# Performance work log

Hardware: AMD Instinct MI355X
Metric: run time of the kernel (lower is better)

## Reference

```python
import jax, jax.numpy as jnp
import numpy as np

BSZ, SEQ, DIM, NH = 2, 2048, 2048, 16
HD = DIM // NH  # 128


def setup_inputs() -> dict:
    key = jax.random.key(0)
    ks = jax.random.split(key, 6)
    x = jax.random.normal(ks[0], (BSZ, SEQ, DIM), dtype=jnp.float32)
    # torch Linear weights: [out_features, in_features]
    scale = 1.0 / np.sqrt(DIM)
    wq = jax.random.normal(ks[1], (DIM, DIM), dtype=jnp.float32) * scale
    wk = jax.random.normal(ks[2], (DIM, DIM), dtype=jnp.float32) * scale
    wv = jax.random.normal(ks[3], (DIM, DIM), dtype=jnp.float32) * scale
    wo = jax.random.normal(ks[4], (DIM, DIM), dtype=jnp.float32) * scale
    # RoPE freqs (llama style): theta=10000
    inv_freq = 1.0 / (10000.0 ** (jnp.arange(0, HD, 2, dtype=jnp.float32) / HD))  # [HD//2]
    t = jnp.arange(SEQ, dtype=jnp.float32)
    angles = jnp.outer(t, inv_freq)  # [SEQ, HD//2]
    freqs_cos = jnp.cos(angles)
    freqs_sin = jnp.sin(angles)
    # causal additive mask [SEQ, SEQ]
    mask = jnp.where(jnp.tril(jnp.ones((SEQ, SEQ), dtype=bool)), 0.0, -jnp.inf).astype(jnp.float32)
    return {"x": x, "wq": wq, "wk": wk, "wv": wv, "wo": wo,
            "freqs_cos": freqs_cos, "freqs_sin": freqs_sin, "mask": mask}


def _apply_rope(v, cos, sin):
    # v: [b, s, h, hd]; complex pairs are interleaved (even=real, odd=imag)
    b, s, h, hd = v.shape
    vr = v.reshape(b, s, h, hd // 2, 2)
    v0, v1 = vr[..., 0], vr[..., 1]
    c = cos[None, :, None, :]  # [1, s, 1, hd//2]
    sn = sin[None, :, None, :]
    out = jnp.stack([v0 * c - v1 * sn, v0 * sn + v1 * c], axis=-1)
    return out.reshape(b, s, h, hd)


def reference(x, wq, wk, wv, wo, freqs_cos, freqs_sin, mask):
    b, s, _ = x.shape
    xq = (x @ wq.T).reshape(b, s, NH, HD)
    xk = (x @ wk.T).reshape(b, s, NH, HD)
    xv = (x @ wv.T).reshape(b, s, NH, HD)
    xq = _apply_rope(xq, freqs_cos, freqs_sin)
    xk = _apply_rope(xk, freqs_cos, freqs_sin)
    # [b, h, s, s]
    scores = jnp.einsum('bqhd,bkhd->bhqk', xq, xk) / jnp.sqrt(jnp.float32(HD))
    scores = scores + mask[None, None, :, :]
    probs = jax.nn.softmax(scores.astype(jnp.float32), axis=-1).astype(scores.dtype)
    out = jnp.einsum('bhqk,bkhd->bqhd', probs, xv).reshape(b, s, NH * HD)
    return out @ wo.T
```

## Files before the change

### kernel.cpp

```cpp
#include <hip/hip_runtime.h>
#include <hip/hip_bf16.h>
#include <stdint.h>

typedef __bf16 bf16x8 __attribute__((ext_vector_type(8)));
typedef float f32x4 __attribute__((ext_vector_type(4)));
typedef unsigned short u16;
typedef unsigned int u32;

#define DEVI __device__ __forceinline__

DEVI u16 f2b(float f){ __bf16 h = (__bf16)f; return __builtin_bit_cast(u16, h); }
DEVI float b2f(u16 u){ return (float)__builtin_bit_cast(__bf16, u); }

constexpr int BSZ = 2, SEQ = 2048, DIM = 2048, NH = 16, HD = 128;

#if defined(__has_builtin)
#if __has_builtin(__builtin_amdgcn_global_load_lds)
#define HAVE_ASYNC_LDS 1
#endif
#endif

DEVI void cp16(void* lds, const void* g){
#ifdef HAVE_ASYNC_LDS
  auto gp = (const __attribute__((address_space(1))) u32*)(uintptr_t)g;
  auto lp = (__attribute__((address_space(3))) u32*)(uintptr_t)lds;
  __builtin_amdgcn_global_load_lds(gp, lp, 16, 0, 0);
#else
  *(uint4*)lds = *(const uint4*)g;
#endif
}

__global__ __launch_bounds__(256) void k_convert(
    const float* __restrict__ x, const float* __restrict__ wq,
    const float* __restrict__ wk, const float* __restrict__ wv,
    const float* __restrict__ wo,
    u16* __restrict__ xb, u16* __restrict__ wqkv, u16* __restrict__ wob)
{
  int e = (blockIdx.x * 256 + threadIdx.x) * 4;
  float4 v; u16* dp;
  if (e < 8388608){
    v = *(const float4*)&x[e]; dp = &xb[e];
  } else if (e < 20971520){
    int o = e - 8388608; int sec = o >> 22; int oo = o & 4194303;
    const float* w = (sec == 0) ? wq : ((sec == 1) ? wk : wv);
    v = *(const float4*)&w[oo]; dp = &wqkv[o];
  } else {
    int o = e - 20971520;
    v = *(const float4*)&wo[o]; dp = &wob[o];
  }
  ushort4 r; r.x = f2b(v.x); r.y = f2b(v.y); r.z = f2b(v.z); r.w = f2b(v.w);
  *(ushort4*)dp = r;
}

__global__ __launch_bounds__(256) void k_gemm_qkv(
    const u16* __restrict__ A, const u16* __restrict__ W,
    const float* __restrict__ fc, const float* __restrict__ fs,
    u16* __restrict__ Qd, u16* __restrict__ Kd, u16* __restrict__ Vd)
{
  __shared__ u16 As[128*32];
  __shared__ u16 Bs[128*32];
  __shared__ u16 Cs[128*136];
  const int t = threadIdx.x;
  const int lane = t & 63;
  const int l15 = lane & 15, quad = lane >> 4;
  const int wave = t >> 6;
  const int wr = (wave >> 1) * 64, wc = (wave & 1) * 64;
  const int tm = blockIdx.y * 128, tn = blockIdx.x * 128;
  const int arow = t >> 2, acol = (t & 3) * 8;

  f32x4 acc[4][4] = {};
  for (int k0 = 0; k0 < DIM; k0 += 32){
    __syncthreads();
    #pragma unroll
    for (int is = 0; is < 2; ++is){
      int row = is*64 + arow;
      cp16(&As[is*2048 + t*8], &A[(size_t)(tm + row)*DIM + k0 + acol]);
      cp16(&Bs[is*2048 + t*8], &W[(size_t)(tn + row)*DIM + k0 + acol]);
    }
    __syncthreads();
    bf16x8 af[4], bfr[4];
    #pragma unroll
    for (int i = 0; i < 4; ++i){
      af[i]  = *(const bf16x8*)&As[(wr + i*16 + l15)*32 + quad*8];
      bfr[i] = *(const bf16x8*)&Bs[(wc + i*16 + l15)*32 + quad*8];
    }
    #pragma unroll
    for (int mt = 0; mt < 4; ++mt)
      #pragma unroll
      for (int nt = 0; nt < 4; ++nt)
        acc[mt][nt] = __builtin_amdgcn_mfma_f32_16x16x32_bf16(af[mt], bfr[nt], acc[mt][nt], 0, 0, 0);
  }
  #pragma unroll
  for (int mt = 0; mt < 4; ++mt)
    #pragma unroll
    for (int nt = 0; nt < 4; ++nt)
      #pragma unroll
      for (int r = 0; r < 4; ++r)
        Cs[(wr + mt*16 + quad*4 + r)*136 + wc + nt*16 + l15] = f2b(acc[mt][nt][r]);
  __syncthreads();

  const int sec = tn >> 11;
  const int hh = (tn & 2047) >> 7;
  u16* dst = (sec == 0) ? Qd : ((sec == 1) ? Kd : Vd);
  const float qs = (sec == 0) ? (0.08838834764831845f * 1.4426950408889634f) : 1.0f;
  const int col0 = (t & 15) * 8;
  #pragma unroll
  for (int jj = 0; jj < 8; ++jj){
    int row = (t >> 4) + jj*16;
    int m = tm + row;
    int b = m >> 11, s = m & 2047;
    uint4 cv = *(const uint4*)&Cs[row*136 + col0];
    const u16* cp = (const u16*)&cv;
    u16 op[8];
    if (sec < 2){
      float4 c4 = *(const float4*)&fc[(size_t)s*64 + (col0 >> 1)];
      float4 s4 = *(const float4*)&fs[(size_t)s*64 + (col0 >> 1)];
      float cc[4] = {c4.x*qs, c4.y*qs, c4.z*qs, c4.w*qs};
      float ss[4] = {s4.x*qs, s4.y*qs, s4.z*qs, s4.w*qs};
      #pragma unroll
      for (int p = 0; p < 4; ++p){
        float a = b2f(cp[2*p]), bb = b2f(cp[2*p+1]);
        op[2*p]   = f2b(a*cc[p] - bb*ss[p]);
        op[2*p+1] = f2b(a*ss[p] + bb*cc[p]);
      }
    } else {
      #pragma unroll
      for (int p = 0; p < 8; ++p) op[p] = cp[p];
    }
    *(uint4*)&dst[((size_t)(b*NH + hh)*SEQ + s)*HD + col0] = *(const uint4*)op;
  }
}

__global__ __launch_bounds__(256) void k_vtrans(
    const u16* __restrict__ V, u16* __restrict__ Vt)
{
  __shared__ u16 ts[64*72];
  const int t = threadIdx.x;
  const int st = blockIdx.x, dt = blockIdx.y, bh = blockIdx.z;
  const size_t base  = (size_t)bh * SEQ * HD;
  const size_t baseT = (size_t)bh * HD * SEQ;
  #pragma unroll
  for (int i = 0; i < 2; ++i){
    int s = i*32 + (t>>3), c = t&7;
    *(uint4*)&ts[s*72 + c*8] = *(const uint4*)&V[base + (size_t)(st*64 + s)*HD + dt*64 + c*8];
  }
  __syncthreads();
  #pragma unroll
  for (int i = 0; i < 2; ++i){
    int d = i*32 + (t>>3), sc = t&7;
    u16 tmp[8];
    #pragma unroll
    for (int j = 0; j < 8; ++j) tmp[j] = ts[(sc*8 + j)*72 + d];
    *(uint4*)&Vt[baseT + (size_t)(dt*64 + d)*SEQ + st*64 + sc*8] = *(const uint4*)tmp;
  }
}

__global__ __launch_bounds__(512) void k_flash(
    const u16* __restrict__ Qd, const u16* __restrict__ Kd,
    const u16* __restrict__ Vt, u16* __restrict__ OP0, u16* __restrict__ OP1,
    float* __restrict__ Mp, float* __restrict__ Lp)
{
  __shared__ u16 Ks[64*136];
  __shared__ u16 Vs[128*72];
  __shared__ u16 Ps[8*16*72];

  const int t = threadIdx.x, lane = t & 63, wave = t >> 6;
  const int l15 = lane & 15, quad = lane >> 4;
  const int j = blockIdx.x >> 1, split = blockIdx.x & 1;
  const int h = blockIdx.y, b = blockIdx.z, bh = b*NH + h;
  const size_t base  = (size_t)bh * SEQ * HD;
  const size_t baseT = (size_t)bh * HD * SEQ;
  u16* Psw = &Ps[wave*16*72];
  u16* OPs = split ? OP1 : OP0;
  const int lo = 17*split, hi = lo + 17;
  const int qt0 = j, qt1 = 15 - j;
  const int len0 = 2*qt0 + 2;

  const int krow = t >> 4, kcol = (t & 15) * 8;
  const int vrow = t >> 3, vcol = (t & 7) * 8;

  for (int pass = 0; pass < 2; ++pass){
    const int qt = pass ? qt1 : qt0;
    const int len = 2*qt + 2;
    int kt0 = pass ? (lo - len0) : lo; if (kt0 < 0) kt0 = 0;
    int kt1 = pass ? (hi - len0) : hi; if (kt1 > len) kt1 = len;
    const int qb = qt*128 + wave*16;

    bf16x8 qf[4];
    #pragma unroll
    for (int ks = 0; ks < 4; ++ks)
      qf[ks] = *(const bf16x8*)&Qd[base + (size_t)(qb + l15)*HD + ks*32 + quad*8];

    f32x4 oacc[8] = {};
    float m_s = -1e30f, l_s = 0.f;

    if (kt0 < kt1){
      uint4 kreg[2], vreg[2];
      #pragma unroll
      for (int i = 0; i < 2; ++i){
        kreg[i] = *(const uint4*)&Kd[base + (size_t)(kt0*64 + i*32 + krow)*HD + kcol];
        vreg[i] = *(const uint4*)&Vt[baseT + (size_t)(i*64 + vrow)*SEQ + kt0*64 + vcol];
      }
      for (int kt = kt0; kt < kt1; ++kt){
        __syncthreads();
        #pragma unroll
        for (int i = 0; i < 2; ++i){
          *(uint4*)&Ks[(i*32 + krow)*136 + kcol] = kreg[i];
          *(uint4*)&Vs[(i*64 + vrow)*72 + vcol] = vreg[i];
        }
        __syncthreads();
        if (kt + 1 < kt1){
          #pragma unroll
          for (int i = 0; i < 2; ++i){
            kreg[i] = *(const uint4*)&Kd[base + (size_t)((kt+1)*64 + i*32 + krow)*HD + kcol];
            vreg[i] = *(const uint4*)&Vt[baseT + (size_t)(i*64 + vrow)*SEQ + (kt+1)*64 + vcol];
          }
        }
        if (kt*64 <= qb + 15){
          f32x4 sacc[4] = {};
          #pragma unroll
          for (int ks = 0; ks < 4; ++ks){
            bf16x8 kf[4];
            #pragma unroll
            for (int nk = 0; nk < 4; ++nk)
              kf[nk] = *(const bf16x8*)&Ks[(nk*16 + l15)*136 + ks*32 + quad*8];
            #pragma unroll
            for (int nk = 0; nk < 4; ++nk)
              sacc[nk] = __builtin_amdgcn_mfma_f32_16x16x32_bf16(kf[nk], qf[ks], sacc[nk], 0, 0, 0);
          }
          if (kt*64 + 63 > qb){
            int q = qb + l15;
            #pragma unroll
            for (int nk = 0; nk < 4; ++nk)
              #pragma unroll
              for (int r = 0; r < 4; ++r){
                int key = kt*64 + nk*16 + quad*4 + r;
                if (key > q) sacc[nk][r] = -1e30f;
              }
          }
          float m4[4];
          #pragma unroll
          for (int nk = 0; nk < 4; ++nk)
            m4[nk] = fmaxf(fmaxf(sacc[nk][0], sacc[nk][1]), fmaxf(sacc[nk][2], sacc[nk][3]));
          float rm = fmaxf(fmaxf(m4[0], m4[1]), fmaxf(m4[2], m4[3]));
          rm = fmaxf(rm, __shfl_xor(rm, 16));
          rm = fmaxf(rm, __shfl_xor(rm, 32));
          float mnew = fmaxf(m_s, rm);
          float alpha = exp2f(m_s - mnew);
          m_s = mnew;
          float s4[4];
          #pragma unroll
          for (int nk = 0; nk < 4; ++nk){
            u16 pk[4];
            float p0 = exp2f(sacc[nk][0] - mnew);
            float p1 = exp2f(sacc[nk][1] - mnew);
            float p2 = exp2f(sacc[nk][2] - mnew);
            float p3 = exp2f(sacc[nk][3] - mnew);
            pk[0] = f2b(p0); pk[1] = f2b(p1); pk[2] = f2b(p2); pk[3] = f2b(p3);
            s4[nk] = (p0 + p1) + (p2 + p3);
            *(uint2*)&Psw[l15*72 + nk*16 + quad*4] = *(const uint2*)pk;
          }
          float rs = (s4[0] + s4[1]) + (s4[2] + s4[3]);
          rs += __shfl_xor(rs, 16);
          rs += __shfl_xor(rs, 32);
          l_s = l_s*alpha + rs;
          #pragma unroll
          for (int db = 0; db < 8; ++db)
            #pragma unroll
            for (int r = 0; r < 4; ++r) oacc[db][r] *= alpha;
          #pragma unroll
          for (int k2 = 0; k2 < 2; ++k2){
            bf16x8 pf = *(const bf16x8*)&Psw[l15*72 + k2*32 + quad*8];
            #pragma unroll
            for (int db = 0; db < 8; ++db){
              bf16x8 vf = *(const bf16x8*)&Vs[(db*16 + l15)*72 + k2*32 + quad*8];
              oacc[db] = __builtin_amdgcn_mfma_f32_16x16x32_bf16(vf, pf, oacc[db], 0, 0, 0);
            }
          }
        }
      }
    }
    {
      int s = qb + l15;
      #pragma unroll
      for (int db = 0; db < 8; ++db){
        u16 ok[4];
        #pragma unroll
        for (int r = 0; r < 4; ++r) ok[r] = f2b(oacc[db][r]);
        *(uint2*)&OPs[(((size_t)(b*SEQ + s))*NH + h)*HD + db*16 + quad*4] = *(const uint2*)ok;
      }
      if (quad == 0){
        size_t mi = ((size_t)split*BSZ*NH + bh)*SEQ + s;
        Mp[mi] = m_s;
        Lp[mi] = l_s;
      }
    }
  }
}

__global__ __launch_bounds__(256) void k_combine(
    u16* __restrict__ OP0, const u16* __restrict__ OP1,
    const float* __restrict__ Mp, const float* __restrict__ Lp)
{
  size_t flat = ((size_t)blockIdx.x*256 + threadIdx.x)*8;
  int h = (int)((flat >> 7) & 15);
  int s = (int)((flat >> 11) & 2047);
  int b = (int)(flat >> 22);
  size_t row = ((size_t)(b*NH + h))*SEQ + s;
  const size_t off1 = (size_t)BSZ*NH*SEQ;
  float m0 = Mp[row], l0 = Lp[row];
  float m1 = Mp[row + off1], l1 = Lp[row + off1];
  float m = fmaxf(m0, m1);
  float w0 = exp2f(m0 - m), w1 = exp2f(m1 - m);
  float inv = 1.0f / (w0*l0 + w1*l1);
  uint4 a = *(const uint4*)&OP0[flat];
  uint4 c = *(const uint4*)&OP1[flat];
  const u16* pa = (const u16*)&a;
  const u16* pc = (const u16*)&c;
  u16 o[8];
  #pragma unroll
  for (int i = 0; i < 8; ++i)
    o[i] = f2b((b2f(pa[i])*w0 + b2f(pc[i])*w1) * inv);
  *(uint4*)&OP0[flat] = *(const uint4*)o;
}

__global__ __launch_bounds__(256) void k_gemm_out(
    const u16* __restrict__ A, const u16* __restrict__ W, float* __restrict__ out)
{
  __shared__ u16 As[128*32];
  __shared__ u16 Bs[128*32];
  const int t = threadIdx.x;
  const int lane = t & 63;
  const int l15 = lane & 15, quad = lane >> 4;
  const int wave = t >> 6;
  const int wr = (wave >> 1) * 64, wc = (wave & 1) * 64;
  const int tm = blockIdx.y * 128, tn = blockIdx.x * 128;
  const int arow = t >> 2, acol = (t & 3) * 8;

  f32x4 acc[4][4] = {};
  for (int k0 = 0; k0 < DIM; k0 += 32){
    __syncthreads();
    #pragma unroll
    for (int is = 0; is < 2; ++is){
      int row = is*64 + arow;
      cp16(&As[is*2048 + t*8], &A[(size_t)(tm + row)*DIM + k0 + acol]);
      cp16(&Bs[is*2048 + t*8], &W[(size_t)(tn + row)*DIM + k0 + acol]);
    }
    __syncthreads();
    bf16x8 af[4], bfr[4];
    #pragma unroll
    for (int i = 0; i < 4; ++i){
      af[i]  = *(const bf16x8*)&As[(wr + i*16 + l15)*32 + quad*8];
      bfr[i] = *(const bf16x8*)&Bs[(wc + i*16 + l15)*32 + quad*8];
    }
    #pragma unroll
    for (int mt = 0; mt < 4; ++mt)
      #pragma unroll
      for (int nt = 0; nt < 4; ++nt)
        acc[mt][nt] = __builtin_amdgcn_mfma_f32_16x16x32_bf16(af[mt], bfr[nt], acc[mt][nt], 0, 0, 0);
  }
  #pragma unroll
  for (int mt = 0; mt < 4; ++mt)
    #pragma unroll
    for (int nt = 0; nt < 4; ++nt)
      #pragma unroll
      for (int r = 0; r < 4; ++r){
        int row = tm + wr + mt*16 + quad*4 + r;
        int col = tn + wc + nt*16 + l15;
        out[(size_t)row*DIM + col] = acc[mt][nt][r];
      }
}

extern "C" void kernel_launch(void* const* d_in, const int* in_sizes, int n_in,
                              void* d_out, int out_size, void* d_ws, size_t ws_size,
                              hipStream_t stream)
{
  const float* x  = (const float*)d_in[0];
  const float* wq = (const float*)d_in[1];
  const float* wk = (const float*)d_in[2];
  const float* wv = (const float*)d_in[3];
  const float* wo = (const float*)d_in[4];
  const float* fc = (const float*)d_in[5];
  const float* fs = (const float*)d_in[6];
  float* out = (float*)d_out;

  char* ws = (char*)d_ws;
  u16* xb   = (u16*)(ws);
  u16* wqkv = (u16*)(ws + 16777216);
  u16* wob  = (u16*)(ws + 41943040);
  u16* Qr   = (u16*)(ws + 50331648);
  u16* Kr   = (u16*)(ws + 67108864);
  u16* Vr   = (u16*)(ws + 83886080);
  u16* Ob   = (u16*)(ws + 100663296);
  u16* VtT  = xb;
  u16* OP1  = wqkv;
  float* Mp = (float*)(ws + 33554432);
  float* Lp = (float*)(ws + 34078720);

  k_convert <<<24576, 256, 0, stream>>>(x, wq, wk, wv, wo, xb, wqkv, wob);
  k_gemm_qkv<<<dim3(48, 32), 256, 0, stream>>>(xb, wqkv, fc, fs, Qr, Kr, Vr);
  k_vtrans  <<<dim3(32, 2, 32), 256, 0, stream>>>(Vr, VtT);
  k_flash   <<<dim3(16, NH, BSZ), 512, 0, stream>>>(Qr, Kr, VtT, Ob, OP1, Mp, Lp);
  k_combine <<<4096, 256, 0, stream>>>(Ob, OP1, Mp, Lp);
  k_gemm_out<<<dim3(16, 32), 256, 0, stream>>>(Ob, wob, out);
}
```

Baseline: 467.2 us.

## Rewrite projection GEMMs with 256x128 tiles, double-buffered K=64 staging and swizzled LDS

Both projection GEMMs now share one core with 256x128 tiles on 512 threads. Global-to-LDS copies are double-buffered over K steps of 64, which removes one barrier per iteration and overlaps loads with MFMA work. LDS is XOR-swizzled to avoid bank conflicts, MFMA bursts are raised in priority, and block ids are remapped so neighbouring workgroups share input tiles in cache. The output GEMM launches only 256 blocks, which may underfill the GPU and hurt occupancy.

New measurement: 434.5 us. 7.0% less time.

```diff
diff --git a/kernel.cpp b/kernel.cpp
--- a/kernel.cpp
+++ b/kernel.cpp
@@ -52,51 +52,92 @@
   *(ushort4*)dp = r;
 }
 
-__global__ __launch_bounds__(256) void k_gemm_qkv(
+DEVI void gemm_core_256x128(u16* smem, const u16* __restrict__ A, const u16* __restrict__ B,
+                            int tm, int tn, int t, f32x4 (&acc)[4][4])
+{
+  const int lane = t & 63, l15 = lane & 15, quad = lane >> 4;
+  const int wave = t >> 6, wm = wave >> 1, wn = wave & 1;
+  const int swr = (l15 & 7) << 3;
+  const int rb = t >> 3;
+  const int csw = ((t & 7) ^ (rb & 7)) << 3;
+  const u16* As0 = A + (size_t)(tm + rb) * DIM + csw;
+  const u16* Bs0 = B + (size_t)(tn + rb) * DIM + csw;
+
+  auto STAGE = [&](int kt){
+    const int buf = kt & 1;
+    const int kb = kt * 64;
+    u16* d = &smem[buf * 24576 + t * 8];
+    #pragma unroll
+    for (int p = 0; p < 4; ++p)
+      cp16(d + p * 4096, As0 + (size_t)p * (64 * DIM) + kb);
+    #pragma unroll
+    for (int p = 0; p < 2; ++p)
+      cp16(d + 16384 + p * 4096, Bs0 + (size_t)p * (64 * DIM) + kb);
+  };
+
+  STAGE(0);
+  #pragma unroll 2
+  for (int kt = 0; kt < DIM / 64; ++kt){
+    __syncthreads();
+    if (kt < DIM / 64 - 1) STAGE(kt + 1);
+    const u16* Ab = &smem[(kt & 1) * 24576];
+    const u16* Bb = Ab + 16384;
+    bf16x8 Af[4][2], Bf[4][2];
+    #pragma unroll
+    for (int mt = 0; mt < 4; ++mt)
+      #pragma unroll
+      for (int ks = 0; ks < 2; ++ks)
+        Af[mt][ks] = *(const bf16x8*)&Ab[(wm * 64 + mt * 16 + l15) * 64 + ((ks * 32 + quad * 8) ^ swr)];
+    #pragma unroll
+    for (int nt = 0; nt < 4; ++nt)
+      #pragma unroll
+      for (int ks = 0; ks < 2; ++ks)
+        Bf[nt][ks] = *(const bf16x8*)&Bb[(wn * 64 + nt * 16 + l15) * 64 + ((ks * 32 + quad * 8) ^ swr)];
+    #pragma unroll
+    for (int c = 0; c < 4; ++c){
+      const int mb = (c >> 1) * 2, nb = (c & 1) * 2;
+      __builtin_amdgcn_s_setprio(1);
+      #pragma unroll
+      for (int mi = 0; mi < 2; ++mi)
+        #pragma unroll
+        for (int ni = 0; ni < 2; ++ni)
+          #pragma unroll
+          for (int ks = 0; ks < 2; ++ks)
+            acc[mb + mi][nb + ni] = __builtin_amdgcn_mfma_f32_16x16x32_bf16(
+                Af[mb + mi][ks], Bf[nb + ni][ks], acc[mb + mi][nb + ni], 0, 0, 0);
+      __builtin_amdgcn_s_setprio(0);
+    }
+  }
+  __syncthreads();
+}
+
+__global__ __launch_bounds__(512, 2) void k_gemm_qkv(
     const u16* __restrict__ A, const u16* __restrict__ W,
     const float* __restrict__ fc, const float* __restrict__ fs,
     u16* __restrict__ Qd, u16* __restrict__ Kd, u16* __restrict__ Vd)
 {
-  __shared__ u16 As[128*32];
-  __shared__ u16 Bs[128*32];
-  __shared__ u16 Cs[128*136];
+  __shared__ __align__(16) u16 smem[49152];
   const int t = threadIdx.x;
-  const int lane = t & 63;
-  const int l15 = lane & 15, quad = lane >> 4;
-  const int wave = t >> 6;
-  const int wr = (wave >> 1) * 64, wc = (wave & 1) * 64;
-  const int tm = blockIdx.y * 128, tn = blockIdx.x * 128;
-  const int arow = t >> 2, acol = (t & 3) * 8;
-
+  const int wg = blockIdx.x;
+  const int id = (wg & 7) * 96 + (wg >> 3);
+  const int tm = (id & 15) << 8;
+  const int tn = (id >> 4) << 7;
   f32x4 acc[4][4] = {};
-  for (int k0 = 0; k0 < DIM; k0 += 32){
-    __syncthreads();
-    #pragma unroll
-    for (int is = 0; is < 2; ++is){
-      int row = is*64 + arow;
-      cp16(&As[is*2048 + t*8], &A[(size_t)(tm + row)*DIM + k0 + acol]);
-      cp16(&Bs[is*2048 + t*8], &W[(size_t)(tn + row)*DIM + k0 + acol]);
-    }
-    __syncthreads();
-    bf16x8 af[4], bfr[4];
-    #pragma unroll
-    for (int i = 0; i < 4; ++i){
-      af[i]  = *(const bf16x8*)&As[(wr + i*16 + l15)*32 + quad*8];
-      bfr[i] = *(const bf16x8*)&Bs[(wc + i*16 + l15)*32 + quad*8];
-    }
-    #pragma unroll
-    for (int mt = 0; mt < 4; ++mt)
-      #pragma unroll
-      for (int nt = 0; nt < 4; ++nt)
-        acc[mt][nt] = __builtin_amdgcn_mfma_f32_16x16x32_bf16(af[mt], bfr[nt], acc[mt][nt], 0, 0, 0);
-  }
+  gemm_core_256x128(smem, A, W, tm, tn, t, acc);
+
+  const int lane = t & 63, l15 = lane & 15, quad = lane >> 4;
+  const int wave = t >> 6, wm = wave >> 1, wn = wave & 1;
+  u16* Cs = smem;
   #pragma unroll
   for (int mt = 0; mt < 4; ++mt)
     #pragma unroll
     for (int nt = 0; nt < 4; ++nt)
       #pragma unroll
-      for (int r = 0; r < 4; ++r)
-        Cs[(wr + mt*16 + quad*4 + r)*136 + wc + nt*16 + l15] = f2b(acc[mt][nt][r]);
+      for (int r = 0; r < 4; ++r){
+        int rin = wm * 64 + mt * 16 + quad * 4 + r;
+        int col = wn * 64 + nt * 16 + l15;
+        Cs[rin * 128 + ((col + rin * 8) & 127)] = f2b(acc[mt][nt][r]);
+      }
   __syncthreads();
 
   const int sec = tn >> 11;
@@ -106,15 +147,15 @@
   const int col0 = (t & 15) * 8;
   #pragma unroll
   for (int jj = 0; jj < 8; ++jj){
-    int row = (t >> 4) + jj*16;
+    int row = (t >> 4) + jj * 32;
     int m = tm + row;
     int b = m >> 11, s = m & 2047;
-    uint4 cv = *(const uint4*)&Cs[row*136 + col0];
+    uint4 cv = *(const uint4*)&Cs[row * 128 + ((col0 + row * 8) & 127)];
     const u16* cp = (const u16*)&cv;
     u16 op[8];
     if (sec < 2){
-      float4 c4 = *(const float4*)&fc[(size_t)s*64 + (col0 >> 1)];
-      float4 s4 = *(const float4*)&fs[(size_t)s*64 + (col0 >> 1)];
+      float4 c4 = *(const float4*)&fc[(size_t)s * 64 + (col0 >> 1)];
+      float4 s4 = *(const float4*)&fs[(size_t)s * 64 + (col0 >> 1)];
       float cc[4] = {c4.x*qs, c4.y*qs, c4.z*qs, c4.w*qs};
       float ss[4] = {s4.x*qs, s4.y*qs, s4.z*qs, s4.w*qs};
       #pragma unroll
@@ -324,49 +365,27 @@
   *(uint4*)&OP0[flat] = *(const uint4*)o;
 }
 
-__global__ __launch_bounds__(256) void k_gemm_out(
+__global__ __launch_bounds__(512, 2) void k_gemm_out(
     const u16* __restrict__ A, const u16* __restrict__ W, float* __restrict__ out)
 {
-  __shared__ u16 As[128*32];
-  __shared__ u16 Bs[128*32];
+  __shared__ __align__(16) u16 smem[49152];
   const int t = threadIdx.x;
-  const int lane = t & 63;
-  const int l15 = lane & 15, quad = lane >> 4;
-  const int wave = t >> 6;
-  const int wr = (wave >> 1) * 64, wc = (wave & 1) * 64;
-  const int tm = blockIdx.y * 128, tn = blockIdx.x * 128;
-  const int arow = t >> 2, acol = (t & 3) * 8;
-
+  const int wg = blockIdx.x;
+  const int id = (wg & 7) * 32 + (wg >> 3);
+  const int tm = (id & 15) << 8;
+  const int tn = (id >> 4) << 7;
   f32x4 acc[4][4] = {};
-  for (int k0 = 0; k0 < DIM; k0 += 32){
-    __syncthreads();
-    #pragma unroll
-    for (int is = 0; is < 2; ++is){
-      int row = is*64 + arow;
-      cp16(&As[is*2048 + t*8], &A[(size_t)(tm + row)*DIM + k0 + acol]);
-      cp16(&Bs[is*2048 + t*8], &W[(size_t)(tn + row)*DIM + k0 + acol]);
-    }
-    __syncthreads();
-    bf16x8 af[4], bfr[4];
-    #pragma unroll
-    for (int i = 0; i < 4; ++i){
-      af[i]  = *(const bf16x8*)&As[(wr + i*16 + l15)*32 + quad*8];
-      bfr[i] = *(const bf16x8*)&Bs[(wc + i*16 + l15)*32 + quad*8];
-    }
-    #pragma unroll
-    for (int mt = 0; mt < 4; ++mt)
-      #pragma unroll
-      for (int nt = 0; nt < 4; ++nt)
-        acc[mt][nt] = __builtin_amdgcn_mfma_f32_16x16x32_bf16(af[mt], bfr[nt], acc[mt][nt], 0, 0, 0);
-  }
+  gemm_core_256x128(smem, A, W, tm, tn, t, acc);
+  const int lane = t & 63, l15 = lane & 15, quad = lane >> 4;
+  const int wave = t >> 6, wm = wave >> 1, wn = wave & 1;
   #pragma unroll
   for (int mt = 0; mt < 4; ++mt)
     #pragma unroll
     for (int nt = 0; nt < 4; ++nt)
       #pragma unroll
       for (int r = 0; r < 4; ++r){
-        int row = tm + wr + mt*16 + quad*4 + r;
-        int col = tn + wc + nt*16 + l15;
+        int row = tm + wm*64 + mt*16 + quad*4 + r;
+        int col = tn + wn*64 + nt*16 + l15;
         out[(size_t)row*DIM + col] = acc[mt][nt][r];
       }
 }
@@ -398,9 +417,9 @@
   float* Lp = (float*)(ws + 34078720);
 
   k_convert <<<24576, 256, 0, stream>>>(x, wq, wk, wv, wo, xb, wqkv, wob);
-  k_gemm_qkv<<<dim3(48, 32), 256, 0, stream>>>(xb, wqkv, fc, fs, Qr, Kr, Vr);
+  k_gemm_qkv<<<768, 512, 0, stream>>>(xb, wqkv, fc, fs, Qr, Kr, Vr);
   k_vtrans  <<<dim3(32, 2, 32), 256, 0, stream>>>(Vr, VtT);
   k_flash   <<<dim3(16, NH, BSZ), 512, 0, stream>>>(Qr, Kr, VtT, Ob, OP1, Mp, Lp);
   k_combine <<<4096, 256, 0, stream>>>(Ob, OP1, Mp, Lp);
-  k_gemm_out<<<dim3(16, 32), 256, 0, stream>>>(Ob, wob, out);
-}
+  k_gemm_out<<<256, 512, 0, stream>>>(Ob, wob, out);
+}
```
